# Optimization experiments

Hardware: AMD Instinct MI355X
Metric: run time of the kernel (lower is better)

Reference implementation:

```python
import jax, jax.numpy as jnp
import numpy as np

N = 16384

def setup_inputs() -> dict:
    key = jax.random.key(0)
    k1, k2, k3 = jax.random.split(key, 3)
    hazard_pred = jax.random.normal(k1, (N, 1), dtype=jnp.float32)
    durations = jax.random.uniform(k2, (N,), dtype=jnp.float32)
    events = jax.random.uniform(k3, (N,), dtype=jnp.float32)
    return {"hazard_pred": hazard_pred, "durations": durations, "events": events}

def reference(hazard_pred, durations, events):
    theta = hazard_pred.reshape(-1)                      # [n]
    # risk-set mask: R[i, j] = durations[j] >= durations[i]
    R = (durations[None, :] >= durations[:, None]).astype(theta.dtype)  # [n, n]
    # sum_j exp(theta_j) * R[i, j]  -> fused masked row-sum (single GEMV)
    risk_sum = R @ jnp.exp(theta)                        # [n]
    loss_cox = -jnp.mean((theta - jnp.log(risk_sum)) * events)
    return loss_cox
```

## Files before the change

kernel.cpp:

```cpp
#include <hip/hip_runtime.h>
#include <math.h>

#define NB    2048
#define BLK   256
#define SCANT 1024


__device__ __forceinline__ int bucket_of(float d) {
    int b = (int)(d * (float)NB);
    return min(max(b, 0), NB - 1);
}

__global__ __launch_bounds__(BLK)
void zero_kernel(int* __restrict__ ws_i) {
    int i = blockIdx.x * BLK + threadIdx.x;
    if (i < 4098) ws_i[i] = 0;
}

__global__ __launch_bounds__(BLK)
void stats_kernel(const float* __restrict__ hazard,
                  const float* __restrict__ durations,
                  float* __restrict__ sumExp, int* __restrict__ cnt, int n) {
    int j = blockIdx.x * BLK + threadIdx.x;
    if (j >= n) return;
    float d = durations[j];
    float e = expf(hazard[j]);
    int b = bucket_of(d);
    atomicAdd(&sumExp[b], e);
    atomicAdd(&cnt[b], 1);
}

__global__ __launch_bounds__(SCANT)
void scan_kernel(const float* __restrict__ sumExp, const int* __restrict__ cnt,
                 int* __restrict__ offsets, int* __restrict__ cursor,
                 float* __restrict__ suffixGT) {
    __shared__ float fa[NB], fb[NB];
    __shared__ int   ia[NB], ib[NB];
    const int tid = threadIdx.x;

    #pragma unroll
    for (int k = 0; k < NB / SCANT; ++k) {
        int idx = tid + k * SCANT;
        fa[idx] = sumExp[NB - 1 - idx];
        ia[idx] = cnt[idx];
    }
    __syncthreads();

    bool pa = true;
    for (int d = 1; d < NB; d <<= 1) {
        #pragma unroll
        for (int k = 0; k < NB / SCANT; ++k) {
            int idx = tid + k * SCANT;
            float fsrc = pa ? fa[idx] : fb[idx];
            int   isrc = pa ? ia[idx] : ib[idx];
            float fadd = (idx >= d) ? (pa ? fa[idx - d] : fb[idx - d]) : 0.0f;
            int   iadd = (idx >= d) ? (pa ? ia[idx - d] : ib[idx - d]) : 0;
            if (pa) { fb[idx] = fsrc + fadd; ib[idx] = isrc + iadd; }
            else    { fa[idx] = fsrc + fadd; ia[idx] = isrc + iadd; }
        }
        __syncthreads();
        pa = !pa;
    }
    #pragma unroll
    for (int k = 0; k < NB / SCANT; ++k) {
        int idx = tid + k * SCANT;
        int iexcl = (idx > 0) ? (pa ? ia[idx - 1] : ib[idx - 1]) : 0;
        offsets[idx] = iexcl;
        cursor[idx]  = iexcl;
        suffixGT[idx] = (idx + 1 < NB) ? (pa ? fa[NB - 2 - idx] : fb[NB - 2 - idx]) : 0.0f;
    }
}

__global__ __launch_bounds__(BLK)
void scatter_kernel(const float* __restrict__ hazard,
                    const float* __restrict__ durations,
                    const int* __restrict__ offsets,
                    int* __restrict__ cursor,
                    float2* __restrict__ sorted, int n) {
    int j = blockIdx.x * BLK + threadIdx.x;
    if (j >= n) return;
    float d = durations[j];
    float e = expf(hazard[j]);
    int b = bucket_of(d);
    int pos = atomicAdd(&cursor[b], 1);
    sorted[pos] = make_float2(d, e);
}

__global__ __launch_bounds__(BLK)
void loss_kernel(const float* __restrict__ hazard,
                 const float* __restrict__ durations,
                 const float* __restrict__ events,
                 const int* __restrict__ offsets, const int* __restrict__ cnt,
                 const float* __restrict__ suffixGT,
                 const float2* __restrict__ sorted,
                 float* __restrict__ wsum, int* __restrict__ done,
                 float* __restrict__ out, int n) {
    const int i = blockIdx.x * BLK + threadIdx.x;
    float d = durations[i];
    int b = bucket_of(d);
    float s = suffixGT[b];
    int off = offsets[b], c = cnt[b];
    for (int k = 0; k < c; ++k) {
        float2 v = sorted[off + k];
        s += (v.x >= d) ? v.y : 0.0f;
    }
    float local = (hazard[i] - logf(s)) * events[i];

    #pragma unroll
    for (int o = 32; o > 0; o >>= 1)
        local += __shfl_down(local, o, 64);

    __shared__ float wpart[BLK / 64];
    if ((threadIdx.x & 63) == 0) wpart[threadIdx.x >> 6] = local;
    __syncthreads();
    if (threadIdx.x == 0) {
        float t = 0.0f;
        #pragma unroll
        for (int w = 0; w < BLK / 64; ++w) t += wpart[w];
        atomicAdd(wsum, t);
        __threadfence();
        int ticket = atomicAdd(done, 1);
        if (ticket == (int)gridDim.x - 1) {
            float tot = atomicAdd(wsum, 0.0f);
            out[0] = -tot / (float)n;
        }
    }
}

extern "C" void kernel_launch(void* const* d_in, const int* in_sizes, int n_in,
                              void* d_out, int out_size, void* d_ws, size_t ws_size,
                              hipStream_t stream) {
    const float* hazard    = (const float*)d_in[0];
    const float* durations = (const float*)d_in[1];
    const float* events    = (const float*)d_in[2];
    float* out = (float*)d_out;
    const int n = in_sizes[1];

    char* ws = (char*)d_ws;
    float*  sumExp   = (float*)(ws + 0);
    int*    cnt      = (int*)  (ws + 8192);
    float*  wsum     = (float*)(ws + 16384);
    int*    done     = (int*)  (ws + 16388);
    int*    offsets  = (int*)  (ws + 16640);
    int*    cursor   = (int*)  (ws + 24832);
    float*  suffixGT = (float*)(ws + 33024);
    float2* sorted   = (float2*)(ws + 41216);

    const int nblk = (n + BLK - 1) / BLK;

    zero_kernel   <<<17, BLK, 0, stream>>>((int*)ws);
    stats_kernel  <<<nblk, BLK, 0, stream>>>(hazard, durations, sumExp, cnt, n);
    scan_kernel   <<<1, SCANT, 0, stream>>>(sumExp, cnt, offsets, cursor, suffixGT);
    scatter_kernel<<<nblk, BLK, 0, stream>>>(hazard, durations, offsets, cursor, sorted, n);
    loss_kernel   <<<nblk, BLK, 0, stream>>>(hazard, durations, events, offsets, cnt,
                                             suffixGT, sorted, wsum, done, out, n);
}
```

Baseline: 76.64 us.

## Fuse zero, histogram, scan and scatter into one single-block prep kernel

Replaces the zero, stats, scan and scatter kernels with one 1024-thread block. It builds the bucket histogram in shared-memory atomics, scans it with wave shuffles instead of a log-step shared-memory ping-pong, and scatters the (duration, exp) pairs using a shared cursor. This removes three kernel launches and the global atomics, at the cost of doing all 16384 elements' histogram and scatter work on a single CU. It also hardcodes n = 16 × 1024 and assumes n is a multiple of the block size.

```diff
diff --git a/kernel.cpp b/kernel.cpp
--- a/kernel.cpp
+++ b/kernel.cpp
@@ -1,9 +1,10 @@
 #include <hip/hip_runtime.h>
 #include <math.h>
 
-#define NB    2048
-#define BLK   256
-#define SCANT 1024
+#define NB  2048
+#define PT  1024
+#define EPT 16
+#define BLK 256
 
 
 __device__ __forceinline__ int bucket_of(float d) {
@@ -11,86 +12,96 @@
     return min(max(b, 0), NB - 1);
 }
 
-__global__ __launch_bounds__(BLK)
-void zero_kernel(int* __restrict__ ws_i) {
-    int i = blockIdx.x * BLK + threadIdx.x;
-    if (i < 4098) ws_i[i] = 0;
-}
+__global__ __launch_bounds__(PT)
+void prep_kernel(const float* __restrict__ hazard,
+                 const float* __restrict__ durations,
+                 int* __restrict__ offsets, int* __restrict__ cntArr,
+                 float* __restrict__ suffixGT,
+                 float* __restrict__ wsum, int* __restrict__ done,
+                 float2* __restrict__ sorted, int n) {
+    __shared__ float histF[NB];
+    __shared__ int   histC[NB];
+    __shared__ int   curL[NB];
+    __shared__ float wtF[16];
+    __shared__ int   wtC[16];
+    const int tid  = threadIdx.x;
+    const int lane = tid & 63;
+    const int wv   = tid >> 6;
 
-__global__ __launch_bounds__(BLK)
-void stats_kernel(const float* __restrict__ hazard,
-                  const float* __restrict__ durations,
-                  float* __restrict__ sumExp, int* __restrict__ cnt, int n) {
-    int j = blockIdx.x * BLK + threadIdx.x;
-    if (j >= n) return;
-    float d = durations[j];
-    float e = expf(hazard[j]);
-    int b = bucket_of(d);
-    atomicAdd(&sumExp[b], e);
-    atomicAdd(&cnt[b], 1);
-}
+    histF[tid] = 0.0f; histF[tid + PT] = 0.0f;
+    histC[tid] = 0;    histC[tid + PT] = 0;
+    __syncthreads();
 
-__global__ __launch_bounds__(SCANT)
-void scan_kernel(const float* __restrict__ sumExp, const int* __restrict__ cnt,
-                 int* __restrict__ offsets, int* __restrict__ cursor,
-                 float* __restrict__ suffixGT) {
-    __shared__ float fa[NB], fb[NB];
-    __shared__ int   ia[NB], ib[NB];
-    const int tid = threadIdx.x;
-
+    float dv[EPT], ev[EPT];
     #pragma unroll
-    for (int k = 0; k < NB / SCANT; ++k) {
-        int idx = tid + k * SCANT;
-        fa[idx] = sumExp[NB - 1 - idx];
-        ia[idx] = cnt[idx];
+    for (int k = 0; k < EPT; ++k) {
+        int i = tid + k * PT;
+        dv[k] = durations[i];
+        ev[k] = expf(hazard[i]);
+        int b = bucket_of(dv[k]);
+        atomicAdd(&histF[b], ev[k]);
+        atomicAdd(&histC[b], 1);
     }
     __syncthreads();
 
-    bool pa = true;
-    for (int d = 1; d < NB; d <<= 1) {
+    int   c0 = histC[2 * tid], c1 = histC[2 * tid + 1];
+    float f0 = histF[NB - 1 - 2 * tid];
+    float f1 = histF[NB - 2 - 2 * tid];
+    int   cp = c0 + c1;
+    float fp = f0 + f1;
+    #pragma unroll
+    for (int o = 1; o < 64; o <<= 1) {
+        int   cu = __shfl_up(cp, o, 64);
+        float fu = __shfl_up(fp, o, 64);
+        if (lane >= o) { cp += cu; fp += fu; }
+    }
+    if (lane == 63) { wtC[wv] = cp; wtF[wv] = fp; }
+    __syncthreads();
+    if (wv == 0) {
+        int   c = (lane < 16) ? wtC[lane] : 0;
+        float f = (lane < 16) ? wtF[lane] : 0.0f;
         #pragma unroll
-        for (int k = 0; k < NB / SCANT; ++k) {
-            int idx = tid + k * SCANT;
-            float fsrc = pa ? fa[idx] : fb[idx];
-            int   isrc = pa ? ia[idx] : ib[idx];
-            float fadd = (idx >= d) ? (pa ? fa[idx - d] : fb[idx - d]) : 0.0f;
-            int   iadd = (idx >= d) ? (pa ? ia[idx - d] : ib[idx - d]) : 0;
-            if (pa) { fb[idx] = fsrc + fadd; ib[idx] = isrc + iadd; }
-            else    { fa[idx] = fsrc + fadd; ia[idx] = isrc + iadd; }
+        for (int o = 1; o < 16; o <<= 1) {
+            int   cu = __shfl_up(c, o, 64);
+            float fu = __shfl_up(f, o, 64);
+            if (lane >= o) { c += cu; f += fu; }
         }
-        __syncthreads();
-        pa = !pa;
+        if (lane < 16) { wtC[lane] = c; wtF[lane] = f; }
     }
+    __syncthreads();
+    int   cbase = (wv > 0) ? wtC[wv - 1] : 0;
+    float fbase = (wv > 0) ? wtF[wv - 1] : 0.0f;
+    int   cI1 = cbase + cp;
+    int   cI0 = cI1 - c1;
+    float fI1 = fbase + fp;
+    float fI0 = fI1 - f1;
+
+    int b0 = 2 * tid, b1 = 2 * tid + 1;
+    int e0 = cI0 - c0, e1 = cI1 - c1;
+    offsets[b0] = e0;  offsets[b1] = e1;
+    curL[b0]    = e0;  curL[b1]    = e1;
+    cntArr[b0]  = c0;  cntArr[b1]  = c1;
+    suffixGT[NB - 2 - 2 * tid] = fI0;
+    {
+        int bb = NB - 3 - 2 * tid;
+        if (bb >= 0) suffixGT[bb] = fI1;
+    }
+    if (tid == 0) { suffixGT[NB - 1] = 0.0f; wsum[0] = 0.0f; done[0] = 0; }
+    __syncthreads();
+
     #pragma unroll
-    for (int k = 0; k < NB / SCANT; ++k) {
-        int idx = tid + k * SCANT;
-        int iexcl = (idx > 0) ? (pa ? ia[idx - 1] : ib[idx - 1]) : 0;
-        offsets[idx] = iexcl;
-        cursor[idx]  = iexcl;
-        suffixGT[idx] = (idx + 1 < NB) ? (pa ? fa[NB - 2 - idx] : fb[NB - 2 - idx]) : 0.0f;
+    for (int k = 0; k < EPT; ++k) {
+        int b = bucket_of(dv[k]);
+        int pos = atomicAdd(&curL[b], 1);
+        sorted[pos] = make_float2(dv[k], ev[k]);
     }
-}
-
-__global__ __launch_bounds__(BLK)
-void scatter_kernel(const float* __restrict__ hazard,
-                    const float* __restrict__ durations,
-                    const int* __restrict__ offsets,
-                    int* __restrict__ cursor,
-                    float2* __restrict__ sorted, int n) {
-    int j = blockIdx.x * BLK + threadIdx.x;
-    if (j >= n) return;
-    float d = durations[j];
-    float e = expf(hazard[j]);
-    int b = bucket_of(d);
-    int pos = atomicAdd(&cursor[b], 1);
-    sorted[pos] = make_float2(d, e);
 }
 
 __global__ __launch_bounds__(BLK)
 void loss_kernel(const float* __restrict__ hazard,
                  const float* __restrict__ durations,
                  const float* __restrict__ events,
-                 const int* __restrict__ offsets, const int* __restrict__ cnt,
+                 const int* __restrict__ offsets, const int* __restrict__ cntArr,
                  const float* __restrict__ suffixGT,
                  const float2* __restrict__ sorted,
                  float* __restrict__ wsum, int* __restrict__ done,
@@ -99,7 +110,7 @@
     float d = durations[i];
     int b = bucket_of(d);
     float s = suffixGT[b];
-    int off = offsets[b], c = cnt[b];
+    int off = offsets[b], c = cntArr[b];
     for (int k = 0; k < c; ++k) {
         float2 v = sorted[off + k];
         s += (v.x >= d) ? v.y : 0.0f;
@@ -137,21 +148,16 @@
     const int n = in_sizes[1];
 
     char* ws = (char*)d_ws;
-    float*  sumExp   = (float*)(ws + 0);
-    int*    cnt      = (int*)  (ws + 8192);
-    float*  wsum     = (float*)(ws + 16384);
-    int*    done     = (int*)  (ws + 16388);
-    int*    offsets  = (int*)  (ws + 16640);
-    int*    cursor   = (int*)  (ws + 24832);
-    float*  suffixGT = (float*)(ws + 33024);
-    float2* sorted   = (float2*)(ws + 41216);
+    int*    offsets  = (int*)  (ws + 0);
+    int*    cntArr   = (int*)  (ws + 8192);
+    float*  suffixGT = (float*)(ws + 16384);
+    float*  wsum     = (float*)(ws + 24576);
+    int*    done     = (int*)  (ws + 24580);
+    float2* sorted   = (float2*)(ws + 24832);
 
-    const int nblk = (n + BLK - 1) / BLK;
-
-    zero_kernel   <<<17, BLK, 0, stream>>>((int*)ws);
-    stats_kernel  <<<nblk, BLK, 0, stream>>>(hazard, durations, sumExp, cnt, n);
-    scan_kernel   <<<1, SCANT, 0, stream>>>(sumExp, cnt, offsets, cursor, suffixGT);
-    scatter_kernel<<<nblk, BLK, 0, stream>>>(hazard, durations, offsets, cursor, sorted, n);
-    loss_kernel   <<<nblk, BLK, 0, stream>>>(hazard, durations, events, offsets, cnt,
-                                             suffixGT, sorted, wsum, done, out, n);
+    prep_kernel<<<1, PT, 0, stream>>>(hazard, durations, offsets, cntArr,
+                                      suffixGT, wsum, done, sorted, n);
+    loss_kernel<<<dim3(n / BLK), BLK, 0, stream>>>(hazard, durations, events,
+                                                   offsets, cntArr, suffixGT,
+                                                   sorted, wsum, done, out, n);
 }
```

New measurement: 95.41 us. 1.25x slower.
